# Kernel tuning notes

Measured on AMD Instinct MI355X. Metric: run time of the kernel, lower is better.

The kernel has to match this reference:

```python
import jax, jax.numpy as jnp
import numpy as np

N = 50000; E = 800000; IN = 64; HID = 128; H = 8; C = 16; G = 64
NEG = 0.2  # leaky_relu negative slope (GATv2 default and explicit in forward)

def _ln(x, g, b, eps=1e-5):
    mu = jnp.mean(x, -1, keepdims=True)
    var = jnp.var(x, -1, keepdims=True)
    return (x - mu) * jax.lax.rsqrt(var + eps) * g + b

def _prelu(x, a):
    return jnp.where(x >= 0, x, a * x)

def _gatv2(h, src, dst, Wl, bl, Wr, br, att, bias):
    # GATv2Conv: heads=H, out=C per head, concat=True, add_self_loops=True
    n = h.shape[0]
    loop = jnp.arange(n, dtype=src.dtype)
    s = jnp.concatenate([src, loop]); d = jnp.concatenate([dst, loop])
    xl = (h @ Wl + bl).reshape(n, H, C)   # source transform (messages)
    xr = (h @ Wr + br).reshape(n, H, C)   # target transform
    z = jax.nn.leaky_relu(xl[s] + xr[d], NEG)          # [Etot,H,C]
    e = jnp.einsum('ehc,hc->eh', z, att)               # [Etot,H]
    m = jax.ops.segment_max(e, d, num_segments=n)      # scatter-softmax over dst
    w = jnp.exp(e - m[d])
    denom = jax.ops.segment_sum(w, d, num_segments=n)
    alpha = w / (denom[d] + 1e-16)
    out = jax.ops.segment_sum(xl[s] * alpha[:, :, None], d, num_segments=n)
    return out.reshape(n, H * C) + bias

def _sage(h, src, dst, Wp, bp, Wl, bl, Wr):
    # SAGEConv(aggr='mean', normalize=True, project=True)
    n = h.shape[0]
    xp = jax.nn.relu(h @ Wp + bp)                      # project before aggregation
    summ = jax.ops.segment_sum(xp[src], dst, num_segments=n)
    cnt = jax.ops.segment_sum(jnp.ones_like(dst, dtype=h.dtype), dst, num_segments=n)
    mean = summ / jnp.maximum(cnt, 1.0)[:, None]
    out = mean @ Wl + bl + h @ Wr                      # root uses un-projected h
    nrm = jnp.linalg.norm(out, axis=-1, keepdims=True)
    return out / jnp.maximum(nrm, 1e-12)               # F.normalize(p=2, dim=-1)

def _forward(x, W_in, b_in, W_res, b_res,
             g0_Wl, g0_bl, g0_Wr, g0_br, g0_att, g0_bias,
             s1_Wp, s1_bp, s1_Wl, s1_bl, s1_Wr,
             g2_Wl, g2_bl, g2_Wr, g2_br, g2_att, g2_bias,
             s3_Wp, s3_bp, s3_Wl, s3_bl, s3_Wr,
             ln_g, ln_b, Wap, bap,
             Wc1, bc1, a1, Wc2, bc2, a2, Wc3, bc3,
             edge_index, batch):
    src, dst = edge_index[0], edge_index[1]
    h = (x @ W_in + b_in) + (x @ W_res + b_res)        # input_proj + res_proj
    xs0 = jax.nn.elu(_ln(_gatv2(h, src, dst, g0_Wl, g0_bl, g0_Wr, g0_br, g0_att, g0_bias), ln_g[0], ln_b[0]))
    xs1 = jax.nn.leaky_relu(_ln(_sage(xs0, src, dst, s1_Wp, s1_bp, s1_Wl, s1_bl, s1_Wr), ln_g[1], ln_b[1]), NEG)
    xs2 = jax.nn.elu(_ln(_gatv2(xs1, src, dst, g2_Wl, g2_bl, g2_Wr, g2_br, g2_att, g2_bias), ln_g[2], ln_b[2]))
    xs3 = jax.nn.leaky_relu(_ln(_sage(xs2, src, dst, s3_Wp, s3_bp, s3_Wl, s3_bl, s3_Wr), ln_g[3], ln_b[3]), NEG)
    h = jnp.maximum(jnp.maximum(xs0, xs1), jnp.maximum(xs2, xs3))  # JumpingKnowledge('max')
    att = jax.nn.sigmoid(h @ Wap + bap)
    h = h * att
    summ = jax.ops.segment_sum(h, batch, num_segments=G)
    cnt = jax.ops.segment_sum(jnp.ones((h.shape[0],), h.dtype), batch, num_segments=G)
    pooled = summ / jnp.maximum(cnt, 1.0)[:, None]     # global_mean_pool
    z = _prelu(pooled @ Wc1 + bc1, a1)
    z = _prelu(z @ Wc2 + bc2, a2)
    return z @ Wc3 + bc3

def setup_inputs():
    key = jax.random.key(0)
    ks = iter(jax.random.split(key, 64))
    def nrm(shape, fan):
        return jax.random.normal(next(ks), shape, jnp.float32) / np.sqrt(fan).astype(np.float32)
    inp = {}
    inp['x'] = jax.random.normal(next(ks), (N, IN), jnp.float32)
    inp['edge_index'] = jax.random.randint(next(ks), (2, E), 0, N, jnp.int32)
    inp['batch'] = jnp.sort(jax.random.randint(next(ks), (N,), 0, G, jnp.int32))
    inp['W_in'] = nrm((IN, HID), IN); inp['b_in'] = jnp.zeros((HID,))
    inp['W_res'] = nrm((IN, HID), IN); inp['b_res'] = jnp.zeros((HID,))
    for p in ('g0', 'g2'):
        inp[p + '_Wl'] = nrm((HID, HID), HID); inp[p + '_bl'] = jnp.zeros((HID,))
        inp[p + '_Wr'] = nrm((HID, HID), HID); inp[p + '_br'] = jnp.zeros((HID,))
        inp[p + '_att'] = nrm((H, C), C); inp[p + '_bias'] = jnp.zeros((HID,))
    for p in ('s1', 's3'):
        inp[p + '_Wp'] = nrm((HID, HID), HID); inp[p + '_bp'] = jnp.zeros((HID,))
        inp[p + '_Wl'] = nrm((HID, HID), HID); inp[p + '_bl'] = jnp.zeros((HID,))
        inp[p + '_Wr'] = nrm((HID, HID), HID)
    inp['ln_g'] = jnp.ones((4, HID)); inp['ln_b'] = jnp.zeros((4, HID))
    inp['Wap'] = nrm((HID, 1), HID); inp['bap'] = jnp.zeros((1,))
    inp['Wc1'] = nrm((HID, HID), HID); inp['bc1'] = jnp.zeros((HID,))
    inp['a1'] = jnp.float32(0.25)
    inp['Wc2'] = nrm((HID, HID // 2), HID); inp['bc2'] = jnp.zeros((HID // 2,))
    inp['a2'] = jnp.float32(0.25)
    inp['Wc3'] = nrm((HID // 2, 2), HID // 2); inp['bc3'] = jnp.zeros((2,))
    return inp

def reference(x, edge_index, batch, W_in, b_in, W_res, b_res,
              g0_Wl, g0_bl, g0_Wr, g0_br, g0_att, g0_bias,
              s1_Wp, s1_bp, s1_Wl, s1_bl, s1_Wr,
              g2_Wl, g2_bl, g2_Wr, g2_br, g2_att, g2_bias,
              s3_Wp, s3_bp, s3_Wl, s3_bl, s3_Wr,
              ln_g, ln_b, Wap, bap, Wc1, bc1, a1, Wc2, bc2, a2, Wc3, bc3):
    return _forward(x, W_in, b_in, W_res, b_res,
                    g0_Wl, g0_bl, g0_Wr, g0_br, g0_att, g0_bias,
                    s1_Wp, s1_bp, s1_Wl, s1_bl, s1_Wr,
                    g2_Wl, g2_bl, g2_Wr, g2_br, g2_att, g2_bias,
                    s3_Wp, s3_bp, s3_Wl, s3_bl, s3_Wr,
                    ln_g, ln_b, Wap, bap, Wc1, bc1, a1, Wc2, bc2, a2, Wc3, bc3,
                    edge_index, batch)
```

## Files before the change

kernel.cpp:

```cpp
#include <hip/hip_runtime.h>
#include <math.h>

constexpr int N_ = 50000;
constexpr int E_ = 800000;
constexpr int IN_ = 64;
constexpr int HID_ = 128;
constexpr int G_ = 64;
constexpr float NEG_ = 0.2f;
constexpr float LOG2E_ = 1.44269504088896340736f;

#define ACT_NONE 0
#define ACT_RELU 1

typedef _Float16 half8 __attribute__((ext_vector_type(8)));
typedef _Float16 half2v __attribute__((ext_vector_type(2)));
typedef float floatx4 __attribute__((ext_vector_type(4)));

__global__ __launch_bounds__(256) void hist_kernel(const int* __restrict__ dst,
                                                   int* __restrict__ deg, int e) {
  int i = blockIdx.x * 256 + threadIdx.x;
  if (i < e) atomicAdd(&deg[dst[i]], 1);
}

__global__ __launch_bounds__(256) void scan1_kernel(const int* __restrict__ deg,
                                                    int* __restrict__ excl,
                                                    int* __restrict__ bscan, int n) {
  __shared__ int sh[256];
  int t = threadIdx.x;
  int i = blockIdx.x * 256 + t;
  int v = (i < n) ? deg[i] : 0;
  sh[t] = v;
  __syncthreads();
  for (int off = 1; off < 256; off <<= 1) {
    int y = (t >= off) ? sh[t - off] : 0;
    __syncthreads();
    sh[t] += y;
    __syncthreads();
  }
  int incl = sh[t];
  if (i < n) excl[i] = incl - v;
  if (t == 255) bscan[blockIdx.x] = incl;
}

__global__ __launch_bounds__(256) void scan2_kernel(int* __restrict__ data, int nb) {
  __shared__ int sh[256];
  int t = threadIdx.x;
  int v = (t < nb) ? data[t] : 0;
  sh[t] = v;
  __syncthreads();
  for (int off = 1; off < 256; off <<= 1) {
    int y = (t >= off) ? sh[t - off] : 0;
    __syncthreads();
    sh[t] += y;
    __syncthreads();
  }
  if (t < nb) data[t] = sh[t] - v;
}

__global__ __launch_bounds__(256) void scan3_kernel(int* __restrict__ rowptr,
                                                    int* __restrict__ cursor,
                                                    const int* __restrict__ bscan,
                                                    int n, int e) {
  int i = blockIdx.x * 256 + threadIdx.x;
  if (i < n) {
    int v = rowptr[i] + bscan[blockIdx.x];
    rowptr[i] = v;
    cursor[i] = v;
  }
  if (i == n) rowptr[n] = e;
}

__global__ __launch_bounds__(256) void fill_kernel(const int* __restrict__ src,
                                                   const int* __restrict__ dst,
                                                   int* __restrict__ cursor,
                                                   int* __restrict__ csr, int e) {
  int i = blockIdx.x * 256 + threadIdx.x;
  if (i < e) {
    int d = dst[i];
    int p = atomicAdd(&cursor[d], 1);
    csr[p] = src[i];
  }
}

__global__ __launch_bounds__(256) void addv_kernel(const float* __restrict__ a,
                                                   const float* __restrict__ b,
                                                   float* __restrict__ o, int n) {
  int i = blockIdx.x * 256 + threadIdx.x;
  if (i < n) o[i] = a[i] + b[i];
}

__global__ __launch_bounds__(256) void prep_w_kernel(
    const float* __restrict__ W_in, const float* __restrict__ W_res,
    const float* __restrict__ m0, const float* __restrict__ m1,
    const float* __restrict__ m2, const float* __restrict__ m3,
    const float* __restrict__ m4, const float* __restrict__ m5,
    const float* __restrict__ m6, const float* __restrict__ m7,
    const float* __restrict__ m8, const float* __restrict__ m9,
    _Float16* __restrict__ dst) {
  int idx = blockIdx.x * 256 + threadIdx.x;
  if (idx < 8192) {
    int n = idx >> 6, k = idx & 63;
    float v = W_in[k * 128 + n] + W_res[k * 128 + n];
    _Float16 h = (_Float16)v;
    dst[idx] = h;
    dst[8192 + idx] = (_Float16)(v - (float)h);
  } else if (idx < 8192 + 10 * 16384) {
    int r = idx - 8192;
    int j = r >> 14;
    int e = r & 16383;
    int n = e >> 7, k = e & 127;
    const float* S;
    switch (j) {
      case 0: S = m0; break; case 1: S = m1; break; case 2: S = m2; break;
      case 3: S = m3; break; case 4: S = m4; break; case 5: S = m5; break;
      case 6: S = m6; break; case 7: S = m7; break; case 8: S = m8; break;
      default: S = m9; break;
    }
    float v = S[k * 128 + n];
    _Float16 h = (_Float16)v;
    _Float16* base = dst + 16384 + j * 32768;
    base[e] = h;
    base[16384 + e] = (_Float16)(v - (float)h);
  }
}

__device__ inline void split8v(float4 a, float4 b, half8& h, half8& l) {
  float v0 = a.x, v1 = a.y, v2 = a.z, v3 = a.w;
  float v4 = b.x, v5 = b.y, v6 = b.z, v7 = b.w;
  _Float16 h0 = (_Float16)v0, h1 = (_Float16)v1, h2 = (_Float16)v2, h3 = (_Float16)v3;
  _Float16 h4 = (_Float16)v4, h5 = (_Float16)v5, h6 = (_Float16)v6, h7 = (_Float16)v7;
  h[0] = h0; h[1] = h1; h[2] = h2; h[3] = h3; h[4] = h4; h[5] = h5; h[6] = h6; h[7] = h7;
  l[0] = (_Float16)(v0 - (float)h0); l[1] = (_Float16)(v1 - (float)h1);
  l[2] = (_Float16)(v2 - (float)h2); l[3] = (_Float16)(v3 - (float)h3);
  l[4] = (_Float16)(v4 - (float)h4); l[5] = (_Float16)(v5 - (float)h5);
  l[6] = (_Float16)(v6 - (float)h6); l[7] = (_Float16)(v7 - (float)h7);
}

template <int K1, int ACT, typename OutT>
__global__ __launch_bounds__(256, 2) void gemm_rw(const float* __restrict__ A,
                                                  const _Float16* __restrict__ Wh,
                                                  const _Float16* __restrict__ Wl,
                                                  const float* __restrict__ bias,
                                                  OutT* __restrict__ C, int M) {
  constexpr int KK = K1 / 32;
  const int t = threadIdx.x;
  const int wave = t >> 6, lane = t & 63;
  const int quad = lane >> 4, l16 = lane & 15;
  const int nt0 = wave * 2;

  half8 wh[2][KK], wl[2][KK];
  float bb[2];
  int col[2];
#pragma unroll
  for (int i = 0; i < 2; ++i) {
    col[i] = (nt0 + i) * 16 + l16;
    bb[i] = bias[col[i]];
#pragma unroll
    for (int k = 0; k < KK; ++k) {
      size_t off = (size_t)col[i] * K1 + k * 32 + quad * 8;
      wh[i][k] = *reinterpret_cast<const half8*>(Wh + off);
      wl[i][k] = *reinterpret_cast<const half8*>(Wl + off);
    }
  }
  const int r0 = blockIdx.x * 64;
#pragma unroll
  for (int tt = 0; tt < 4; ++tt) {
    int tb = r0 + tt * 16;
    if (tb >= M) break;
    int arow = tb + l16;
    if (arow >= M) arow = M - 1;
    const float* ap = A + (size_t)arow * K1 + quad * 8;
    float4 a0[KK], a1[KK];
#pragma unroll
    for (int k = 0; k < KK; ++k) {
      a0[k] = *reinterpret_cast<const float4*>(ap + k * 32);
      a1[k] = *reinterpret_cast<const float4*>(ap + k * 32 + 4);
    }
    floatx4 acc[2];
    acc[0] = (floatx4){0.f, 0.f, 0.f, 0.f};
    acc[1] = (floatx4){0.f, 0.f, 0.f, 0.f};
#pragma unroll
    for (int k = 0; k < KK; ++k) {
      half8 ah, al;
      split8v(a0[k], a1[k], ah, al);
      acc[0] = __builtin_amdgcn_mfma_f32_16x16x32_f16(ah, wh[0][k], acc[0], 0, 0, 0);
      acc[0] = __builtin_amdgcn_mfma_f32_16x16x32_f16(ah, wl[0][k], acc[0], 0, 0, 0);
      acc[0] = __builtin_amdgcn_mfma_f32_16x16x32_f16(al, wh[0][k], acc[0], 0, 0, 0);
      acc[1] = __builtin_amdgcn_mfma_f32_16x16x32_f16(ah, wh[1][k], acc[1], 0, 0, 0);
      acc[1] = __builtin_amdgcn_mfma_f32_16x16x32_f16(ah, wl[1][k], acc[1], 0, 0, 0);
      acc[1] = __builtin_amdgcn_mfma_f32_16x16x32_f16(al, wh[1][k], acc[1], 0, 0, 0);
    }
#pragma unroll
    for (int i = 0; i < 2; ++i) {
#pragma unroll
      for (int reg = 0; reg < 4; ++reg) {
        int r = tb + quad * 4 + reg;
        if (r < M) {
          float v = acc[i][reg] + bb[i];
          if (ACT == ACT_RELU) v = fmaxf(v, 0.f);
          C[(size_t)r * 128 + col[i]] = (OutT)v;
        }
      }
    }
  }
}

__global__ __launch_bounds__(256, 2) void gemm_rw_dual_gat(const float* __restrict__ A,
                                                           const _Float16* __restrict__ W0h,
                                                           const _Float16* __restrict__ W0l,
                                                           const _Float16* __restrict__ W1h,
                                                           const _Float16* __restrict__ W1l,
                                                           const float* __restrict__ b0,
                                                           const float* __restrict__ b1,
                                                           _Float16* __restrict__ C0,
                                                           _Float16* __restrict__ C1, int M) {
  const int t = threadIdx.x;
  const int wave = t >> 6, lane = t & 63;
  const int quad = lane >> 4, l16 = lane & 15;
  const int nt0 = wave * 2;

  half8 w0h[2][4], w0l[2][4], w1h[2][4], w1l[2][4];
  float bb0[2], bb1[2];
  int col[2];
#pragma unroll
  for (int i = 0; i < 2; ++i) {
    col[i] = (nt0 + i) * 16 + l16;
    bb0[i] = b0[col[i]];
    bb1[i] = b1[col[i]];
#pragma unroll
    for (int k = 0; k < 4; ++k) {
      size_t off = (size_t)col[i] * 128 + k * 32 + quad * 8;
      w0h[i][k] = *reinterpret_cast<const half8*>(W0h + off);
      w0l[i][k] = *reinterpret_cast<const half8*>(W0l + off);
      w1h[i][k] = *reinterpret_cast<const half8*>(W1h + off);
      w1l[i][k] = *reinterpret_cast<const half8*>(W1l + off);
    }
  }
  const int r0 = blockIdx.x * 64;
#pragma unroll
  for (int tt = 0; tt < 4; ++tt) {
    int tb = r0 + tt * 16;
    if (tb >= M) break;
    int arow = tb + l16;
    if (arow >= M) arow = M - 1;
    const float* ap = A + (size_t)arow * 128 + quad * 8;
    float4 a0[4], a1[4];
#pragma unroll
    for (int k = 0; k < 4; ++k) {
      a0[k] = *reinterpret_cast<const float4*>(ap + k * 32);
      a1[k] = *reinterpret_cast<const float4*>(ap + k * 32 + 4);
    }
    floatx4 acc0[2], acc1[2];
    acc0[0] = (floatx4){0.f, 0.f, 0.f, 0.f};
    acc0[1] = (floatx4){0.f, 0.f, 0.f, 0.f};
    acc1[0] = (floatx4){0.f, 0.f, 0.f, 0.f};
    acc1[1] = (floatx4){0.f, 0.f, 0.f, 0.f};
#pragma unroll
    for (int k = 0; k < 4; ++k) {
      half8 ah, al;
      split8v(a0[k], a1[k], ah, al);
#pragma unroll
      for (int i = 0; i < 2; ++i) {
        acc0[i] = __builtin_amdgcn_mfma_f32_16x16x32_f16(ah, w0h[i][k], acc0[i], 0, 0, 0);
        acc0[i] = __builtin_amdgcn_mfma_f32_16x16x32_f16(ah, w0l[i][k], acc0[i], 0, 0, 0);
        acc0[i] = __builtin_amdgcn_mfma_f32_16x16x32_f16(al, w0h[i][k], acc0[i], 0, 0, 0);
        acc1[i] = __builtin_amdgcn_mfma_f32_16x16x32_f16(ah, w1h[i][k], acc1[i], 0, 0, 0);
        acc1[i] = __builtin_amdgcn_mfma_f32_16x16x32_f16(ah, w1l[i][k], acc1[i], 0, 0, 0);
        acc1[i] = __builtin_amdgcn_mfma_f32_16x16x32_f16(al, w1h[i][k], acc1[i], 0, 0, 0);
      }
    }
#pragma unroll
    for (int i = 0; i < 2; ++i) {
#pragma unroll
      for (int reg = 0; reg < 4; ++reg) {
        int r = tb + quad * 4 + reg;
        if (r < M) {
          C0[(size_t)r * 128 + col[i]] = (_Float16)(acc0[i][reg] + bb0[i]);
          C1[(size_t)r * 128 + col[i]] = (_Float16)(acc1[i][reg] + bb1[i]);
        }
      }
    }
  }
}

__global__ __launch_bounds__(256, 2) void gemm_rw_dual_sage(const float* __restrict__ A1,
                                                            const _Float16* __restrict__ W1h,
                                                            const _Float16* __restrict__ W1l,
                                                            const float* __restrict__ A2,
                                                            const _Float16* __restrict__ W2h,
                                                            const _Float16* __restrict__ W2l,
                                                            const float* __restrict__ bias,
                                                            const float* __restrict__ lng,
                                                            const float* __restrict__ lnb,
                                                            float* __restrict__ C, int M) {
  const int t = threadIdx.x;
  const int wave = t >> 6, lane = t & 63;
  const int quad = lane >> 4, l16 = lane & 15;
  const int nt0 = wave * 2;

  half8 w1h[2][4], w1l[2][4], w2h[2][4], w2l[2][4];
  float bb[2], gg[2], lb[2];
  int col[2];
#pragma unroll
  for (int i = 0; i < 2; ++i) {
    col[i] = (nt0 + i) * 16 + l16;
    bb[i] = bias[col[i]];
    gg[i] = lng[col[i]];
    lb[i] = lnb[col[i]];
#pragma unroll
    for (int k = 0; k < 4; ++k) {
      size_t off = (size_t)col[i] * 128 + k * 32 + quad * 8;
      w1h[i][k] = *reinterpret_cast<const half8*>(W1h + off);
      w1l[i][k] = *reinterpret_cast<const half8*>(W1l + off);
      w2h[i][k] = *reinterpret_cast<const half8*>(W2h + off);
      w2l[i][k] = *reinterpret_cast<const half8*>(W2l + off);
    }
  }
  __shared__ float2 red[2][4][16];
  const int r0 = blockIdx.x * 64;
#pragma unroll 1
  for (int tt = 0; tt < 4; ++tt) {
    int tb = r0 + tt * 16;
    if (tb >= M) break;
    int arow = tb + l16;
    if (arow >= M) arow = M - 1;
    const float* ap1 = A1 + (size_t)arow * 128 + quad * 8;
    const float* ap2 = A2 + (size_t)arow * 128 + quad * 8;
    float4 a0[4], a1[4], c0[4], c1[4];
#pragma unroll
    for (int k = 0; k < 4; ++k) {
      a0[k] = *reinterpret_cast<const float4*>(ap1 + k * 32);
      a1[k] = *reinterpret_cast<const float4*>(ap1 + k * 32 + 4);
      c0[k] = *reinterpret_cast<const float4*>(ap2 + k * 32);
      c1[k] = *reinterpret_cast<const float4*>(ap2 + k * 32 + 4);
    }
    floatx4 acc[2];
    acc[0] = (floatx4){0.f, 0.f, 0.f, 0.f};
    acc[1] = (floatx4){0.f, 0.f, 0.f, 0.f};
#pragma unroll
    for (int k = 0; k < 4; ++k) {
      half8 ah, al;
      split8v(a0[k], a1[k], ah, al);
#pragma unroll
      for (int i = 0; i < 2; ++i) {
        acc[i] = __builtin_amdgcn_mfma_f32_16x16x32_f16(ah, w1h[i][k], acc[i], 0, 0, 0);
        acc[i] = __builtin_amdgcn_mfma_f32_16x16x32_f16(ah, w1l[i][k], acc[i], 0, 0, 0);
        acc[i] = __builtin_amdgcn_mfma_f32_16x16x32_f16(al, w1h[i][k], acc[i], 0, 0, 0);
      }
    }
#pragma unroll
    for (int k = 0; k < 4; ++k) {
      half8 ah, al;
      split8v(c0[k], c1[k], ah, al);
#pragma unroll
      for (int i = 0; i < 2; ++i) {
        acc[i] = __builtin_amdgcn_mfma_f32_16x16x32_f16(ah, w2h[i][k], acc[i], 0, 0, 0);
        acc[i] = __builtin_amdgcn_mfma_f32_16x16x32_f16(ah, w2l[i][k], acc[i], 0, 0, 0);
        acc[i] = __builtin_amdgcn_mfma_f32_16x16x32_f16(al, w2h[i][k], acc[i], 0, 0, 0);
      }
    }
    float v0[4], v1[4], p1[4], p2[4];
#pragma unroll
    for (int reg = 0; reg < 4; ++reg) {
      v0[reg] = acc[0][reg] + bb[0];
      v1[reg] = acc[1][reg] + bb[1];
      p1[reg] = v0[reg] + v1[reg];
      p2[reg] = v0[reg] * v0[reg] + v1[reg] * v1[reg];
    }
#pragma unroll
    for (int off = 1; off < 16; off <<= 1) {
#pragma unroll
      for (int reg = 0; reg < 4; ++reg) {
        p1[reg] += __shfl_xor(p1[reg], off, 64);
        p2[reg] += __shfl_xor(p2[reg], off, 64);
      }
    }
    int par = tt & 1;
    if (l16 == 0) {
#pragma unroll
      for (int reg = 0; reg < 4; ++reg)
        red[par][wave][quad * 4 + reg] = make_float2(p1[reg], p2[reg]);
    }
    __syncthreads();
#pragma unroll
    for (int reg = 0; reg < 4; ++reg) {
      int rr = quad * 4 + reg;
      float2 q0 = red[par][0][rr], q1 = red[par][1][rr];
      float2 q2 = red[par][2][rr], q3 = red[par][3][rr];
      float s1 = q0.x + q1.x + q2.x + q3.x;
      float s2 = q0.y + q1.y + q2.y + q3.y;
      float inv = 1.f / fmaxf(sqrtf(s2), 1e-12f);
      float mu = s1 * inv * (1.f / 128.f);
      float ex2 = (s2 * inv) * inv * (1.f / 128.f);
      float rstd = rsqrtf(ex2 - mu * mu + 1e-5f);
      int r = tb + rr;
      if (r < M) {
        float o0 = (v0[reg] * inv - mu) * rstd * gg[0] + lb[0];
        float o1 = (v1[reg] * inv - mu) * rstd * gg[1] + lb[1];
        o0 = fmaxf(o0, NEG_ * o0);
        o1 = fmaxf(o1, NEG_ * o1);
        C[(size_t)r * 128 + col[0]] = o0;
        C[(size_t)r * 128 + col[1]] = o1;
      }
    }
  }
}

__global__ __launch_bounds__(256) void gat_ln_kernel(const _Float16* __restrict__ xl,
                                                     const _Float16* __restrict__ xr,
                                                     const float* __restrict__ att,
                                                     const float* __restrict__ gbias,
                                                     const int* __restrict__ rowptr,
                                                     const int* __restrict__ csr,
                                                     const float* __restrict__ lng,
                                                     const float* __restrict__ lnb,
                                                     float* __restrict__ out, int n) {
  int wid = (blockIdx.x * 256 + threadIdx.x) >> 6;
  int lane = threadIdx.x & 63;
  if (wid >= n) return;
  const int h = lane >> 3, e = lane & 7;
  const char* __restrict__ xbase = (const char*)(xl + h * 16);

  half2v xr2[8], at2[8];
  {
    const uint4* xrp = reinterpret_cast<const uint4*>(xr + (size_t)wid * 128 + h * 16);
    uint4 u0 = xrp[0], u1 = xrp[1];
    unsigned uu[8] = {u0.x, u0.y, u0.z, u0.w, u1.x, u1.y, u1.z, u1.w};
#pragma unroll
    for (int i = 0; i < 8; ++i) xr2[i] = __builtin_bit_cast(half2v, uu[i]);
    const float2* ap = reinterpret_cast<const float2*>(att + h * 16);
#pragma unroll
    for (int i = 0; i < 8; ++i) {
      float2 a = ap[i];
      at2[i][0] = (_Float16)(a.x * LOG2E_);
      at2[i][1] = (_Float16)(a.y * LOG2E_);
    }
  }
  const half2v negc = {(_Float16)NEG_, (_Float16)NEG_};

  float m0, den;
  float acc[16];
  {
    const uint4* sp = reinterpret_cast<const uint4*>(xbase + (size_t)wid * 256);
    uint4 u0 = sp[0], u1 = sp[1];
    unsigned uu[8] = {u0.x, u0.y, u0.z, u0.w, u1.x, u1.y, u1.z, u1.w};
    float p = 0.f;
#pragma unroll
    for (int i = 0; i < 8; ++i) {
      half2v x = __builtin_bit_cast(half2v, uu[i]);
      half2v z = x + xr2[i];
      half2v zl = __builtin_elementwise_max(z, z * negc);
      p = __builtin_amdgcn_fdot2(zl, at2[i], p, false);
    }
    m0 = p;
    float w = (e == 0) ? 1.f : 0.f;
    den = w;
#pragma unroll
    for (int i = 0; i < 8; ++i) {
      half2v x = __builtin_bit_cast(half2v, uu[i]);
      acc[2 * i] = w * (float)x[0];
      acc[2 * i + 1] = w * (float)x[1];
    }
  }

  int beg = rowptr[wid], end = rowptr[wid + 1];
  for (int base = beg; base < end; base += 8) {
    int idx = base + e;
    bool valid = idx < end;
    int ci = valid ? idx : end - 1;
    int s = csr[ci];
    const uint4* gp = reinterpret_cast<const uint4*>(xbase + (size_t)s * 256);
    uint4 u0 = gp[0], u1 = gp[1];
    unsigned uu[8] = {u0.x, u0.y, u0.z, u0.w, u1.x, u1.y, u1.z, u1.w};
    float p = 0.f;
#pragma unroll
    for (int i = 0; i < 8; ++i) {
      half2v x = __builtin_bit_cast(half2v, uu[i]);
      half2v z = x + xr2[i];
      half2v zl = __builtin_elementwise_max(z, z * negc);
      p = __builtin_amdgcn_fdot2(zl, at2[i], p, false);
    }
    float w = valid ? exp2f(p - m0) : 0.f;
    den += w;
#pragma unroll
    for (int i = 0; i < 8; ++i) {
      half2v x = __builtin_bit_cast(half2v, uu[i]);
      acc[2 * i] += w * (float)x[0];
      acc[2 * i + 1] += w * (float)x[1];
    }
  }

#pragma unroll
  for (int off = 1; off < 8; off <<= 1) {
    den += __shfl_xor(den, off, 64);
#pragma unroll
    for (int i = 0; i < 16; ++i) acc[i] += __shfl_xor(acc[i], off, 64);
  }

  float inv = 1.f / (den + 1e-16f);
  int c = h * 16 + 2 * e;
  float2 bv = reinterpret_cast<const float2*>(gbias + c)[0];
  float o0 = acc[2 * e] * inv + bv.x;
  float o1 = acc[2 * e + 1] * inv + bv.y;
  float s1 = o0 + o1;
  float s2 = o0 * o0 + o1 * o1;
#pragma unroll
  for (int off = 1; off < 64; off <<= 1) {
    s1 += __shfl_xor(s1, off, 64);
    s2 += __shfl_xor(s2, off, 64);
  }
  float mu = s1 * (1.f / 128.f);
  float var = s2 * (1.f / 128.f) - mu * mu;
  float rstd = rsqrtf(var + 1e-5f);
  float2 gvv = reinterpret_cast<const float2*>(lng + c)[0];
  float2 lbv = reinterpret_cast<const float2*>(lnb + c)[0];
  float e0 = (o0 - mu) * rstd * gvv.x + lbv.x;
  float e1 = (o1 - mu) * rstd * gvv.y + lbv.y;
  e0 = e0 > 0.f ? e0 : exp2f(e0 * LOG2E_) - 1.f;
  e1 = e1 > 0.f ? e1 : exp2f(e1 * LOG2E_) - 1.f;
  *reinterpret_cast<float2*>(out + (size_t)wid * 128 + c) = make_float2(e0, e1);
}

__global__ __launch_bounds__(256) void sage_agg_kernel(const _Float16* __restrict__ xp,
                                                       const int* __restrict__ rowptr,
                                                       const int* __restrict__ csr,
                                                       float* __restrict__ mean, int n) {
  int wid = (blockIdx.x * 256 + threadIdx.x) >> 6;
  int lane = threadIdx.x & 63;
  if (wid >= n) return;
  const int g = lane >> 3, e = lane & 7;
  const char* __restrict__ xbase = (const char*)(xp + g * 16);

  float acc[16];
#pragma unroll
  for (int i = 0; i < 16; ++i) acc[i] = 0.f;

  int beg = rowptr[wid], end = rowptr[wid + 1];
  for (int base = beg; base < end; base += 8) {
    int idx = base + e;
    bool valid = idx < end;
    int ci = valid ? idx : end - 1;
    int s = csr[ci];
    const uint4* gp = reinterpret_cast<const uint4*>(xbase + (size_t)s * 256);
    uint4 u0 = gp[0], u1 = gp[1];
    unsigned uu[8] = {u0.x, u0.y, u0.z, u0.w, u1.x, u1.y, u1.z, u1.w};
    float w = valid ? 1.f : 0.f;
#pragma unroll
    for (int i = 0; i < 8; ++i) {
      half2v x = __builtin_bit_cast(half2v, uu[i]);
      acc[2 * i] += w * (float)x[0];
      acc[2 * i + 1] += w * (float)x[1];
    }
  }
#pragma unroll
  for (int off = 1; off < 8; off <<= 1) {
#pragma unroll
    for (int i = 0; i < 16; ++i) acc[i] += __shfl_xor(acc[i], off, 64);
  }
  float inv = 1.f / fmaxf((float)(end - beg), 1.f);
  int c = g * 16 + 2 * e;
  *reinterpret_cast<float2*>(mean + (size_t)wid * 128 + c) =
      make_float2(acc[2 * e] * inv, acc[2 * e + 1] * inv);
}

__global__ __launch_bounds__(256) void jk_pool_kernel(const float* __restrict__ x0,
                                                      const float* __restrict__ x1,
                                                      const float* __restrict__ x2,
                                                      const float* __restrict__ x3,
                                                      const float* __restrict__ wap,
                                                      const float* __restrict__ bap,
                                                      const int* __restrict__ batch,
                                                      float* __restrict__ pooled,
                                                      float* __restrict__ cnt, int n,
                                                      int chunk) {
  int wid = (blockIdx.x * 256 + threadIdx.x) >> 6;
  int lane = threadIdx.x & 63;
  int start = wid * chunk;
  if (start >= n) return;
  int end = start + chunk;
  if (end > n) end = n;

  const float2 wv = reinterpret_cast<const float2*>(wap)[lane];
  const float b0 = bap[0];

  int cur = -1;
  float2 acc = make_float2(0.f, 0.f);
  float c = 0.f;

  for (int i = start; i < end; ++i) {
    int off = i * 64 + lane;
    float2 a0 = reinterpret_cast<const float2*>(x0)[off];
    float2 a1 = reinterpret_cast<const float2*>(x1)[off];
    float2 a2 = reinterpret_cast<const float2*>(x2)[off];
    float2 a3 = reinterpret_cast<const float2*>(x3)[off];
    float2 v;
    v.x = fmaxf(fmaxf(a0.x, a1.x), fmaxf(a2.x, a3.x));
    v.y = fmaxf(fmaxf(a0.y, a1.y), fmaxf(a2.y, a3.y));
    float p = v.x * wv.x + v.y * wv.y;
#pragma unroll
    for (int o = 1; o < 64; o <<= 1) p += __shfl_xor(p, o, 64);
    float a = 1.f / (1.f + exp2f(-(p + b0) * LOG2E_));
    int bg = batch[i];
    if (bg != cur) {
      if (cur >= 0) {
        atomicAdd(&pooled[cur * 128 + 2 * lane], acc.x);
        atomicAdd(&pooled[cur * 128 + 2 * lane + 1], acc.y);
        if (lane == 0) atomicAdd(&cnt[cur], c);
      }
      cur = bg;
      acc = make_float2(0.f, 0.f);
      c = 0.f;
    }
    acc.x += v.x * a;
    acc.y += v.y * a;
    c += 1.f;
  }
  if (cur >= 0) {
    atomicAdd(&pooled[cur * 128 + 2 * lane], acc.x);
    atomicAdd(&pooled[cur * 128 + 2 * lane + 1], acc.y);
    if (lane == 0) atomicAdd(&cnt[cur], c);
  }
}

__global__ __launch_bounds__(128) void mlp_kernel(const float* __restrict__ pooled,
                                                  const float* __restrict__ cnt,
                                                  const float* __restrict__ Wc1,
                                                  const float* __restrict__ bc1,
                                                  const float* __restrict__ a1,
                                                  const float* __restrict__ Wc2,
                                                  const float* __restrict__ bc2,
                                                  const float* __restrict__ a2,
                                                  const float* __restrict__ Wc3,
                                                  const float* __restrict__ bc3,
                                                  float* __restrict__ out) {
  __shared__ float sh[128];
  __shared__ float sh2[128];
  __shared__ float sh3[64];
  int g = blockIdx.x, t = threadIdx.x;
  float inv = 1.f / fmaxf(cnt[g], 1.f);
  sh[t] = pooled[g * 128 + t] * inv;
  __syncthreads();
  float z = bc1[t];
  for (int k = 0; k < 128; ++k) z += sh[k] * Wc1[k * 128 + t];
  float al = a1[0];
  z = z >= 0.f ? z : al * z;
  sh2[t] = z;
  __syncthreads();
  if (t < 64) {
    float z2 = bc2[t];
    for (int k = 0; k < 128; ++k) z2 += sh2[k] * Wc2[k * 64 + t];
    float a2v = a2[0];
    z2 = z2 >= 0.f ? z2 : a2v * z2;
    sh3[t] = z2;
  }
  __syncthreads();
  if (t < 2) {
    float o = bc3[t];
    for (int k = 0; k < 64; ++k) o += sh3[k] * Wc3[k * 2 + t];
    out[g * 2 + t] = o;
  }
}

extern "C" void kernel_launch(void* const* d_in, const int* in_sizes, int n_in,
                              void* d_out, int out_size, void* d_ws, size_t ws_size,
                              hipStream_t stream) {
  const float* x = (const float*)d_in[0];
  const int* ei = (const int*)d_in[1];
  const int* batch = (const int*)d_in[2];
  const float* W_in = (const float*)d_in[3];
  const float* b_in = (const float*)d_in[4];
  const float* W_res = (const float*)d_in[5];
  const float* b_res = (const float*)d_in[6];
  const float* g0_Wl = (const float*)d_in[7];
  const float* g0_bl = (const float*)d_in[8];
  const float* g0_Wr = (const float*)d_in[9];
  const float* g0_br = (const float*)d_in[10];
  const float* g0_att = (const float*)d_in[11];
  const float* g0_bias = (const float*)d_in[12];
  const float* g2_Wl = (const float*)d_in[13];
  const float* g2_bl = (const float*)d_in[14];
  const float* g2_Wr = (const float*)d_in[15];
  const float* g2_br = (const float*)d_in[16];
  const float* g2_att = (const float*)d_in[17];
  const float* g2_bias = (const float*)d_in[18];
  const float* s1_Wp = (const float*)d_in[19];
  const float* s1_bp = (const float*)d_in[20];
  const float* s1_Wl = (const float*)d_in[21];
  const float* s1_bl = (const float*)d_in[22];
  const float* s1_Wr = (const float*)d_in[23];
  const float* s3_Wp = (const float*)d_in[24];
  const float* s3_bp = (const float*)d_in[25];
  const float* s3_Wl = (const float*)d_in[26];
  const float* s3_bl = (const float*)d_in[27];
  const float* s3_Wr = (const float*)d_in[28];
  const float* ln_g = (const float*)d_in[29];
  const float* ln_b = (const float*)d_in[30];
  const float* Wap = (const float*)d_in[31];
  const float* bap = (const float*)d_in[32];
  const float* Wc1 = (const float*)d_in[33];
  const float* bc1 = (const float*)d_in[34];
  const float* a1 = (const float*)d_in[35];
  const float* Wc2 = (const float*)d_in[36];
  const float* bc2 = (const float*)d_in[37];
  const float* a2 = (const float*)d_in[38];
  const float* Wc3 = (const float*)d_in[39];
  const float* bc3 = (const float*)d_in[40];
  float* out = (float*)d_out;

  char* w = (char*)d_ws;
  auto alloc = [&](size_t bytes) -> void* {
    void* p = (void*)w;
    w += (bytes + 255) & ~(size_t)255;
    return p;
  };
  int* deg_cursor = (int*)alloc((size_t)N_ * 4);
  int* rowptr = (int*)alloc((size_t)(N_ + 1) * 4);
  int* bscan = (int*)alloc(256 * 4);
  int* csr = (int*)alloc((size_t)E_ * 4);
  float* bsumf = (float*)alloc((size_t)HID_ * 4);
  float* pooled = (float*)alloc((size_t)G_ * HID_ * 4);
  float* cntf = (float*)alloc((size_t)G_ * 4);
  _Float16* wsp = (_Float16*)alloc((size_t)(16384 + 10 * 32768) * 2);
  size_t big = (size_t)N_ * HID_ * 4;
  size_t bigh = (size_t)N_ * HID_ * 2;
  float* T1 = (float*)alloc(big);
  float* T2 = (float*)alloc(big);
  _Float16* H0 = (_Float16*)alloc(bigh);
  _Float16* H1 = (_Float16*)alloc(bigh);
  float* B0 = (float*)alloc(big);
  float* B1 = (float*)alloc(big);
  float* B2 = (float*)alloc(big);
  float* B3 = (float*)alloc(big);

  const _Float16* WsT_h = wsp;
  const _Float16* WsT_l = wsp + 8192;
  auto WTh = [&](int j) { return (const _Float16*)(wsp + 16384 + j * 32768); };
  auto WTl = [&](int j) { return (const _Float16*)(wsp + 16384 + j * 32768 + 16384); };

  const int EB = (E_ + 255) / 256;
  const int NB256 = (N_ + 255) / 256;
  const int WB = (N_ + 3) / 4;
  const int GB = (N_ + 63) / 64;

  hipMemsetAsync(deg_cursor, 0, (size_t)N_ * 4, stream);
  hist_kernel<<<EB, 256, 0, stream>>>(ei + E_, deg_cursor, E_);
  scan1_kernel<<<NB256, 256, 0, stream>>>(deg_cursor, rowptr, bscan, N_);
  scan2_kernel<<<1, 256, 0, stream>>>(bscan, NB256);
  scan3_kernel<<<NB256, 256, 0, stream>>>(rowptr, deg_cursor, bscan, N_, E_);
  fill_kernel<<<EB, 256, 0, stream>>>(ei, ei + E_, deg_cursor, csr, E_);

  prep_w_kernel<<<(8192 + 10 * 16384 + 255) / 256, 256, 0, stream>>>(
      W_in, W_res, g0_Wl, g0_Wr, s1_Wp, s1_Wl, s1_Wr, g2_Wl, g2_Wr, s3_Wp, s3_Wl, s3_Wr, wsp);
  addv_kernel<<<1, 256, 0, stream>>>(b_in, b_res, bsumf, HID_);

  gemm_rw<64, ACT_NONE, float><<<GB, 256, 0, stream>>>(x, WsT_h, WsT_l, bsumf, T2, N_);

  gemm_rw_dual_gat<<<GB, 256, 0, stream>>>(T2, WTh(0), WTl(0), WTh(1), WTl(1), g0_bl, g0_br,
                                           H0, H1, N_);
  gat_ln_kernel<<<WB, 256, 0, stream>>>(H0, H1, g0_att, g0_bias, rowptr, csr,
                                        ln_g + 0 * 128, ln_b + 0 * 128, B0, N_);

  gemm_rw<128, ACT_RELU, _Float16><<<GB, 256, 0, stream>>>(B0, WTh(2), WTl(2), s1_bp, H0, N_);
  sage_agg_kernel<<<WB, 256, 0, stream>>>(H0, rowptr, csr, T1, N_);
  gemm_rw_dual_sage<<<GB, 256, 0, stream>>>(T1, WTh(3), WTl(3), B0, WTh(4), WTl(4), s1_bl,
                                            ln_g + 1 * 128, ln_b + 1 * 128, B1, N_);

  gemm_rw_dual_gat<<<GB, 256, 0, stream>>>(B1, WTh(5), WTl(5), WTh(6), WTl(6), g2_bl, g2_br,
                                           H0, H1, N_);
  gat_ln_kernel<<<WB, 256, 0, stream>>>(H0, H1, g2_att, g2_bias, rowptr, csr,
                                        ln_g + 2 * 128, ln_b + 2 * 128, B2, N_);

  gemm_rw<128, ACT_RELU, _Float16><<<GB, 256, 0, stream>>>(B2, WTh(7), WTl(7), s3_bp, H0, N_);
  sage_agg_kernel<<<WB, 256, 0, stream>>>(H0, rowptr, csr, T1, N_);
  gemm_rw_dual_sage<<<GB, 256, 0, stream>>>(T1, WTh(8), WTl(8), B2, WTh(9), WTl(9), s3_bl,
                                            ln_g + 3 * 128, ln_b + 3 * 128, B3, N_);

  hipMemsetAsync(pooled, 0, (size_t)G_ * HID_ * 4, stream);
  hipMemsetAsync(cntf, 0, (size_t)G_ * 4, stream);
  {
    const int chunk = 12;
    int nwaves = (N_ + chunk - 1) / chunk;
    int nblocks = (nwaves + 3) / 4;
    jk_pool_kernel<<<nblocks, 256, 0, stream>>>(B0, B1, B2, B3, Wap, bap, batch,
                                                pooled, cntf, N_, chunk);
  }
  mlp_kernel<<<G_, 128, 0, stream>>>(pooled, cntf, Wc1, bc1, a1, Wc2, bc2, a2, Wc3, bc3, out);
}
```

Baseline: 714.5 us.

## Store intermediate activations in fp16 and drop split-precision A operand in GEMMs

All intermediate node feature buffers (T1, T2, B0-B3) now hold fp16 instead of fp32. The GEMMs read fp16 A directly, so they skip the hi/lo split of A and issue two MFMAs per tile instead of three. The bias-add kernel is folded into the weight prep kernel, and the two memsets are merged into one, which assumes pooled and cntf sit next to each other in the allocation. This halves activation memory traffic and cuts MFMA work, at the cost of fp16 rounding of the activations, which may reduce accuracy.

```diff
diff --git a/kernel.cpp b/kernel.cpp
--- a/kernel.cpp
+++ b/kernel.cpp
@@ -82,21 +82,15 @@
   }
 }
 
-__global__ __launch_bounds__(256) void addv_kernel(const float* __restrict__ a,
-                                                   const float* __restrict__ b,
-                                                   float* __restrict__ o, int n) {
-  int i = blockIdx.x * 256 + threadIdx.x;
-  if (i < n) o[i] = a[i] + b[i];
-}
-
 __global__ __launch_bounds__(256) void prep_w_kernel(
     const float* __restrict__ W_in, const float* __restrict__ W_res,
+    const float* __restrict__ b_in, const float* __restrict__ b_res,
     const float* __restrict__ m0, const float* __restrict__ m1,
     const float* __restrict__ m2, const float* __restrict__ m3,
     const float* __restrict__ m4, const float* __restrict__ m5,
     const float* __restrict__ m6, const float* __restrict__ m7,
     const float* __restrict__ m8, const float* __restrict__ m9,
-    _Float16* __restrict__ dst) {
+    _Float16* __restrict__ dst, float* __restrict__ bsum) {
   int idx = blockIdx.x * 256 + threadIdx.x;
   if (idx < 8192) {
     int n = idx >> 6, k = idx & 63;
@@ -121,6 +115,9 @@
     _Float16* base = dst + 16384 + j * 32768;
     base[e] = h;
     base[16384 + e] = (_Float16)(v - (float)h);
+  } else if (idx < 8192 + 10 * 16384 + 128) {
+    int k = idx - (8192 + 10 * 16384);
+    bsum[k] = b_in[k] + b_res[k];
   }
 }
 
@@ -136,13 +133,12 @@
   l[6] = (_Float16)(v6 - (float)h6); l[7] = (_Float16)(v7 - (float)h7);
 }
 
-template <int K1, int ACT, typename OutT>
-__global__ __launch_bounds__(256, 2) void gemm_rw(const float* __restrict__ A,
-                                                  const _Float16* __restrict__ Wh,
-                                                  const _Float16* __restrict__ Wl,
-                                                  const float* __restrict__ bias,
-                                                  OutT* __restrict__ C, int M) {
-  constexpr int KK = K1 / 32;
+__global__ __launch_bounds__(256, 2) void gemm_rw_in(const float* __restrict__ A,
+                                                     const _Float16* __restrict__ Wh,
+                                                     const _Float16* __restrict__ Wl,
+                                                     const float* __restrict__ bias,
+                                                     _Float16* __restrict__ C, int M) {
+  constexpr int K1 = 64, KK = 2;
   const int t = threadIdx.x;
   const int wave = t >> 6, lane = t & 63;
   const int quad = lane >> 4, l16 = lane & 15;
@@ -170,25 +166,78 @@
     int arow = tb + l16;
     if (arow >= M) arow = M - 1;
     const float* ap = A + (size_t)arow * K1 + quad * 8;
-    float4 a0[KK], a1[KK];
-#pragma unroll
-    for (int k = 0; k < KK; ++k) {
-      a0[k] = *reinterpret_cast<const float4*>(ap + k * 32);
-      a1[k] = *reinterpret_cast<const float4*>(ap + k * 32 + 4);
-    }
     floatx4 acc[2];
     acc[0] = (floatx4){0.f, 0.f, 0.f, 0.f};
     acc[1] = (floatx4){0.f, 0.f, 0.f, 0.f};
 #pragma unroll
     for (int k = 0; k < KK; ++k) {
+      float4 a0 = *reinterpret_cast<const float4*>(ap + k * 32);
+      float4 a1 = *reinterpret_cast<const float4*>(ap + k * 32 + 4);
       half8 ah, al;
-      split8v(a0[k], a1[k], ah, al);
+      split8v(a0, a1, ah, al);
       acc[0] = __builtin_amdgcn_mfma_f32_16x16x32_f16(ah, wh[0][k], acc[0], 0, 0, 0);
       acc[0] = __builtin_amdgcn_mfma_f32_16x16x32_f16(ah, wl[0][k], acc[0], 0, 0, 0);
       acc[0] = __builtin_amdgcn_mfma_f32_16x16x32_f16(al, wh[0][k], acc[0], 0, 0, 0);
       acc[1] = __builtin_amdgcn_mfma_f32_16x16x32_f16(ah, wh[1][k], acc[1], 0, 0, 0);
       acc[1] = __builtin_amdgcn_mfma_f32_16x16x32_f16(ah, wl[1][k], acc[1], 0, 0, 0);
       acc[1] = __builtin_amdgcn_mfma_f32_16x16x32_f16(al, wh[1][k], acc[1], 0, 0, 0);
+    }
+#pragma unroll
+    for (int i = 0; i < 2; ++i) {
+#pragma unroll
+      for (int reg = 0; reg < 4; ++reg) {
+        int r = tb + quad * 4 + reg;
+        if (r < M) C[(size_t)r * 128 + col[i]] = (_Float16)(acc[i][reg] + bb[i]);
+      }
+    }
+  }
+}
+
+template <int ACT, typename OutT>
+__global__ __launch_bounds__(256, 2) void gemm_rw16(const _Float16* __restrict__ A,
+                                                    const _Float16* __restrict__ Wh,
+                                                    const _Float16* __restrict__ Wl,
+                                                    const float* __restrict__ bias,
+                                                    OutT* __restrict__ C, int M) {
+  const int t = threadIdx.x;
+  const int wave = t >> 6, lane = t & 63;
+  const int quad = lane >> 4, l16 = lane & 15;
+  const int nt0 = wave * 2;
+
+  half8 wh[2][4], wl[2][4];
+  float bb[2];
+  int col[2];
+#pragma unroll
+  for (int i = 0; i < 2; ++i) {
+    col[i] = (nt0 + i) * 16 + l16;
+    bb[i] = bias[col[i]];
+#pragma unroll
+    for (int k = 0; k < 4; ++k) {
+      size_t off = (size_t)col[i] * 128 + k * 32 + quad * 8;
+      wh[i][k] = *reinterpret_cast<const half8*>(Wh + off);
+      wl[i][k] = *reinterpret_cast<const half8*>(Wl + off);
+    }
+  }
+  const int r0 = blockIdx.x * 64;
+#pragma unroll
+  for (int tt = 0; tt < 4; ++tt) {
+    int tb = r0 + tt * 16;
+    if (tb >= M) break;
+    int arow = tb + l16;
+    if (arow >= M) arow = M - 1;
+    const _Float16* ap = A + (size_t)arow * 128 + quad * 8;
+    half8 a[4];
+#pragma unroll
+    for (int k = 0; k < 4; ++k) a[k] = *reinterpret_cast<const half8*>(ap + k * 32);
+    floatx4 acc[2];
+    acc[0] = (floatx4){0.f, 0.f, 0.f, 0.f};
+    acc[1] = (floatx4){0.f, 0.f, 0.f, 0.f};
+#pragma unroll
+    for (int k = 0; k < 4; ++k) {
+      acc[0] = __builtin_amdgcn_mfma_f32_16x16x32_f16(a[k], wh[0][k], acc[0], 0, 0, 0);
+      acc[0] = __builtin_amdgcn_mfma_f32_16x16x32_f16(a[k], wl[0][k], acc[0], 0, 0, 0);
+      acc[1] = __builtin_amdgcn_mfma_f32_16x16x32_f16(a[k], wh[1][k], acc[1], 0, 0, 0);
+      acc[1] = __builtin_amdgcn_mfma_f32_16x16x32_f16(a[k], wl[1][k], acc[1], 0, 0, 0);
     }
 #pragma unroll
     for (int i = 0; i < 2; ++i) {
@@ -205,15 +254,15 @@
   }
 }
 
-__global__ __launch_bounds__(256, 2) void gemm_rw_dual_gat(const float* __restrict__ A,
-                                                           const _Float16* __restrict__ W0h,
-                                                           const _Float16* __restrict__ W0l,
-                                                           const _Float16* __restrict__ W1h,
-                                                           const _Float16* __restrict__ W1l,
-                                                           const float* __restrict__ b0,
-                                                           const float* __restrict__ b1,
-                                                           _Float16* __restrict__ C0,
-                                                           _Float16* __restrict__ C1, int M) {
+__global__ __launch_bounds__(256, 2) void gemm_rw16_dual_gat(const _Float16* __restrict__ A,
+                                                             const _Float16* __restrict__ W0h,
+                                                             const _Float16* __restrict__ W0l,
+                                                             const _Float16* __restrict__ W1h,
+                                                             const _Float16* __restrict__ W1l,
+                                                             const float* __restrict__ b0,
+                                                             const float* __restrict__ b1,
+                                                             _Float16* __restrict__ C0,
+                                                             _Float16* __restrict__ C1, int M) {
   const int t = threadIdx.x;
   const int wave = t >> 6, lane = t & 63;
   const int quad = lane >> 4, l16 = lane & 15;
@@ -243,13 +292,10 @@
     if (tb >= M) break;
     int arow = tb + l16;
     if (arow >= M) arow = M - 1;
-    const float* ap = A + (size_t)arow * 128 + quad * 8;
-    float4 a0[4], a1[4];
-#pragma unroll
-    for (int k = 0; k < 4; ++k) {
-      a0[k] = *reinterpret_cast<const float4*>(ap + k * 32);
-      a1[k] = *reinterpret_cast<const float4*>(ap + k * 32 + 4);
-    }
+    const _Float16* ap = A + (size_t)arow * 128 + quad * 8;
+    half8 a[4];
+#pragma unroll
+    for (int k = 0; k < 4; ++k) a[k] = *reinterpret_cast<const half8*>(ap + k * 32);
     floatx4 acc0[2], acc1[2];
     acc0[0] = (floatx4){0.f, 0.f, 0.f, 0.f};
     acc0[1] = (floatx4){0.f, 0.f, 0.f, 0.f};
@@ -257,16 +303,12 @@
     acc1[1] = (floatx4){0.f, 0.f, 0.f, 0.f};
 #pragma unroll
     for (int k = 0; k < 4; ++k) {
-      half8 ah, al;
-      split8v(a0[k], a1[k], ah, al);
 #pragma unroll
       for (int i = 0; i < 2; ++i) {
-        acc0[i] = __builtin_amdgcn_mfma_f32_16x16x32_f16(ah, w0h[i][k], acc0[i], 0, 0, 0);
-        acc0[i] = __builtin_amdgcn_mfma_f32_16x16x32_f16(ah, w0l[i][k], acc0[i], 0, 0, 0);
-        acc0[i] = __builtin_amdgcn_mfma_f32_16x16x32_f16(al, w0h[i][k], acc0[i], 0, 0, 0);
-        acc1[i] = __builtin_amdgcn_mfma_f32_16x16x32_f16(ah, w1h[i][k], acc1[i], 0, 0, 0);
-        acc1[i] = __builtin_amdgcn_mfma_f32_16x16x32_f16(ah, w1l[i][k], acc1[i], 0, 0, 0);
-        acc1[i] = __builtin_amdgcn_mfma_f32_16x16x32_f16(al, w1h[i][k], acc1[i], 0, 0, 0);
+        acc0[i] = __builtin_amdgcn_mfma_f32_16x16x32_f16(a[k], w0h[i][k], acc0[i], 0, 0, 0);
+        acc0[i] = __builtin_amdgcn_mfma_f32_16x16x32_f16(a[k], w0l[i][k], acc0[i], 0, 0, 0);
+        acc1[i] = __builtin_amdgcn_mfma_f32_16x16x32_f16(a[k], w1h[i][k], acc1[i], 0, 0, 0);
+        acc1[i] = __builtin_amdgcn_mfma_f32_16x16x32_f16(a[k], w1l[i][k], acc1[i], 0, 0, 0);
       }
     }
 #pragma unroll
@@ -283,16 +325,16 @@
   }
 }
 
-__global__ __launch_bounds__(256, 2) void gemm_rw_dual_sage(const float* __restrict__ A1,
-                                                            const _Float16* __restrict__ W1h,
-                                                            const _Float16* __restrict__ W1l,
-                                                            const float* __restrict__ A2,
-                                                            const _Float16* __restrict__ W2h,
-                                                            const _Float16* __restrict__ W2l,
-                                                            const float* __restrict__ bias,
-                                                            const float* __restrict__ lng,
-                                                            const float* __restrict__ lnb,
-                                                            float* __restrict__ C, int M) {
+__global__ __launch_bounds__(256, 2) void gemm_rw16_dual_sage(const _Float16* __restrict__ A1,
+                                                              const _Float16* __restrict__ W1h,
+                                                              const _Float16* __restrict__ W1l,
+                                                              const _Float16* __restrict__ A2,
+                                                              const _Float16* __restrict__ W2h,
+                                                              const _Float16* __restrict__ W2l,
+                                                              const float* __restrict__ bias,
+                                                              const float* __restrict__ lng,
+                                                              const float* __restrict__ lnb,
+                                                              _Float16* __restrict__ C, int M) {
   const int t = threadIdx.x;
   const int wave = t >> 6, lane = t & 63;
   const int quad = lane >> 4, l16 = lane & 15;
@@ -324,39 +366,25 @@
     if (tb >= M) break;
     int arow = tb + l16;
     if (arow >= M) arow = M - 1;
-    const float* ap1 = A1 + (size_t)arow * 128 + quad * 8;
-    const float* ap2 = A2 + (size_t)arow * 128 + quad * 8;
-    float4 a0[4], a1[4], c0[4], c1[4];
+    const _Float16* ap1 = A1 + (size_t)arow * 128 + quad * 8;
+    const _Float16* ap2 = A2 + (size_t)arow * 128 + quad * 8;
+    half8 a[4], b[4];
 #pragma unroll
     for (int k = 0; k < 4; ++k) {
-      a0[k] = *reinterpret_cast<const float4*>(ap1 + k * 32);
-      a1[k] = *reinterpret_cast<const float4*>(ap1 + k * 32 + 4);
-      c0[k] = *reinterpret_cast<const float4*>(ap2 + k * 32);
-      c1[k] = *reinterpret_cast<const float4*>(ap2 + k * 32 + 4);
+      a[k] = *reinterpret_cast<const half8*>(ap1 + k * 32);
+      b[k] = *reinterpret_cast<const half8*>(ap2 + k * 32);
     }
     floatx4 acc[2];
     acc[0] = (floatx4){0.f, 0.f, 0.f, 0.f};
     acc[1] = (floatx4){0.f, 0.f, 0.f, 0.f};
 #pragma unroll
     for (int k = 0; k < 4; ++k) {
-      half8 ah, al;
-      split8v(a0[k], a1[k], ah, al);
 #pragma unroll
       for (int i = 0; i < 2; ++i) {
-        acc[i] = __builtin_amdgcn_mfma_f32_16x16x32_f16(ah, w1h[i][k], acc[i], 0, 0, 0);
-        acc[i] = __builtin_amdgcn_mfma_f32_16x16x32_f16(ah, w1l[i][k], acc[i], 0, 0, 0);
-        acc[i] = __builtin_amdgcn_mfma_f32_16x16x32_f16(al, w1h[i][k], acc[i], 0, 0, 0);
-      }
-    }
-#pragma unroll
-    for (int k = 0; k < 4; ++k) {
-      half8 ah, al;
-      split8v(c0[k], c1[k], ah, al);
-#pragma unroll
-      for (int i = 0; i < 2; ++i) {
-        acc[i] = __builtin_amdgcn_mfma_f32_16x16x32_f16(ah, w2h[i][k], acc[i], 0, 0, 0);
-        acc[i] = __builtin_amdgcn_mfma_f32_16x16x32_f16(ah, w2l[i][k], acc[i], 0, 0, 0);
-        acc[i] = __builtin_amdgcn_mfma_f32_16x16x32_f16(al, w2h[i][k], acc[i], 0, 0, 0);
+        acc[i] = __builtin_amdgcn_mfma_f32_16x16x32_f16(a[k], w1h[i][k], acc[i], 0, 0, 0);
+        acc[i] = __builtin_amdgcn_mfma_f32_16x16x32_f16(a[k], w1l[i][k], acc[i], 0, 0, 0);
+        acc[i] = __builtin_amdgcn_mfma_f32_16x16x32_f16(b[k], w2h[i][k], acc[i], 0, 0, 0);
+        acc[i] = __builtin_amdgcn_mfma_f32_16x16x32_f16(b[k], w2l[i][k], acc[i], 0, 0, 0);
       }
     }
     float v0[4], v1[4], p1[4], p2[4];
@@ -399,8 +427,8 @@
         float o1 = (v1[reg] * inv - mu) * rstd * gg[1] + lb[1];
         o0 = fmaxf(o0, NEG_ * o0);
         o1 = fmaxf(o1, NEG_ * o1);
-        C[(size_t)r * 128 + col[0]] = o0;
-        C[(size_t)r * 128 + col[1]] = o1;
+        C[(size_t)r * 128 + col[0]] = (_Float16)o0;
+        C[(size_t)r * 128 + col[1]] = (_Float16)o1;
       }
     }
   }
@@ -414,7 +442,7 @@
                                                      const int* __restrict__ csr,
                                                      const float* __restrict__ lng,
                                                      const float* __restrict__ lnb,
-                                                     float* __restrict__ out, int n) {
+                                                     _Float16* __restrict__ out, int n) {
   int wid = (blockIdx.x * 256 + threadIdx.x) >> 6;
   int lane = threadIdx.x & 63;
   if (wid >= n) return;
@@ -518,13 +546,16 @@
   float e1 = (o1 - mu) * rstd * gvv.y + lbv.y;
   e0 = e0 > 0.f ? e0 : exp2f(e0 * LOG2E_) - 1.f;
   e1 = e1 > 0.f ? e1 : exp2f(e1 * LOG2E_) - 1.f;
-  *reinterpret_cast<float2*>(out + (size_t)wid * 128 + c) = make_float2(e0, e1);
+  half2v o;
+  o[0] = (_Float16)e0;
+  o[1] = (_Float16)e1;
+  reinterpret_cast<half2v*>(out)[wid * 64 + (c >> 1)] = o;
 }
 
 __global__ __launch_bounds__(256) void sage_agg_kernel(const _Float16* __restrict__ xp,
                                                        const int* __restrict__ rowptr,
                                                        const int* __restrict__ csr,
-                                                       float* __restrict__ mean, int n) {
+                                                       _Float16* __restrict__ mean, int n) {
   int wid = (blockIdx.x * 256 + threadIdx.x) >> 6;
   int lane = threadIdx.x & 63;
   if (wid >= n) return;
@@ -559,14 +590,16 @@
   }
   float inv = 1.f / fmaxf((float)(end - beg), 1.f);
   int c = g * 16 + 2 * e;
-  *reinterpret_cast<float2*>(mean + (size_t)wid * 128 + c) =
-      make_float2(acc[2 * e] * inv, acc[2 * e + 1] * inv);
-}
-
-__global__ __launch_bounds__(256) void jk_pool_kernel(const float* __restrict__ x0,
-                                                      const float* __restrict__ x1,
-                                                      const float* __restrict__ x2,
-                                                      const float* __restrict__ x3,
+  half2v o;
+  o[0] = (_Float16)(acc[2 * e] * inv);
+  o[1] = (_Float16)(acc[2 * e + 1] * inv);
+  reinterpret_cast<half2v*>(mean)[wid * 64 + (c >> 1)] = o;
+}
+
+__global__ __launch_bounds__(256) void jk_pool_kernel(const _Float16* __restrict__ x0,
+                                                      const _Float16* __restrict__ x1,
+                                                      const _Float16* __restrict__ x2,
+                                                      const _Float16* __restrict__ x3,
                                                       const float* __restrict__ wap,
                                                       const float* __restrict__ bap,
                                                       const int* __restrict__ batch,
@@ -589,13 +622,14 @@
 
   for (int i = start; i < end; ++i) {
     int off = i * 64 + lane;
-    float2 a0 = reinterpret_cast<const float2*>(x0)[off];
-    float2 a1 = reinterpret_cast<const float2*>(x1)[off];
-    float2 a2 = reinterpret_cast<const float2*>(x2)[off];
-    float2 a3 = reinterpret_cast<const float2*>(x3)[off];
-    float2 v;
-    v.x = fmaxf(fmaxf(a0.x, a1.x), fmaxf(a2.x, a3.x));
-    v.y = fmaxf(fmaxf(a0.y, a1.y), fmaxf(a2.y, a3.y));
+    half2v a0 = reinterpret_cast<const half2v*>(x0)[off];
+    half2v a1 = reinterpret_cast<const half2v*>(x1)[off];
+    half2v a2 = reinterpret_cast<const half2v*>(x2)[off];
+    half2v a3 = reinterpret_cast<const half2v*>(x3)[off];
+    half2v m01 = __builtin_elementwise_max(a0, a1);
+    half2v m23 = __builtin_elementwise_max(a2, a3);
+    half2v mm = __builtin_elementwise_max(m01, m23);
+    float2 v = make_float2((float)mm[0], (float)mm[1]);
     float p = v.x * wv.x + v.y * wv.y;
 #pragma unroll
     for (int o = 1; o < 64; o <<= 1) p += __shfl_xor(p, o, 64);
@@ -721,16 +755,15 @@
   float* pooled = (float*)alloc((size_t)G_ * HID_ * 4);
   float* cntf = (float*)alloc((size_t)G_ * 4);
   _Float16* wsp = (_Float16*)alloc((size_t)(16384 + 10 * 32768) * 2);
-  size_t big = (size_t)N_ * HID_ * 4;
   size_t bigh = (size_t)N_ * HID_ * 2;
-  float* T1 = (float*)alloc(big);
-  float* T2 = (float*)alloc(big);
+  _Float16* T1 = (_Float16*)alloc(bigh);
+  _Float16* T2 = (_Float16*)alloc(bigh);
   _Float16* H0 = (_Float16*)alloc(bigh);
   _Float16* H1 = (_Float16*)alloc(bigh);
-  float* B0 = (float*)alloc(big);
-  float* B1 = (float*)alloc(big);
-  float* B2 = (float*)alloc(big);
-  float* B3 = (float*)alloc(big);
+  _Float16* B0 = (_Float16*)alloc(bigh);
+  _Float16* B1 = (_Float16*)alloc(bigh);
+  _Float16* B2 = (_Float16*)alloc(bigh);
+  _Float16* B3 = (_Float16*)alloc(bigh);
 
   const _Float16* WsT_h = wsp;
   const _Float16* WsT_l = wsp + 8192;
@@ -749,34 +782,33 @@
   scan3_kernel<<<NB256, 256, 0, stream>>>(rowptr, deg_cursor, bscan, N_, E_);
   fill_kernel<<<EB, 256, 0, stream>>>(ei, ei + E_, deg_cursor, csr, E_);
 
-  prep_w_kernel<<<(8192 + 10 * 16384 + 255) / 256, 256, 0, stream>>>(
-      W_in, W_res, g0_Wl, g0_Wr, s1_Wp, s1_Wl, s1_Wr, g2_Wl, g2_Wr, s3_Wp, s3_Wl, s3_Wr, wsp);
-  addv_kernel<<<1, 256, 0, stream>>>(b_in, b_res, bsumf, HID_);
-
-  gemm_rw<64, ACT_NONE, float><<<GB, 256, 0, stream>>>(x, WsT_h, WsT_l, bsumf, T2, N_);
-
-  gemm_rw_dual_gat<<<GB, 256, 0, stream>>>(T2, WTh(0), WTl(0), WTh(1), WTl(1), g0_bl, g0_br,
-                                           H0, H1, N_);
+  prep_w_kernel<<<(8192 + 10 * 16384 + 128 + 255) / 256, 256, 0, stream>>>(
+      W_in, W_res, b_in, b_res, g0_Wl, g0_Wr, s1_Wp, s1_Wl, s1_Wr, g2_Wl, g2_Wr, s3_Wp,
+      s3_Wl, s3_Wr, wsp, bsumf);
+
+  gemm_rw_in<<<GB, 256, 0, stream>>>(x, WsT_h, WsT_l, bsumf, T2, N_);
+
+  gemm_rw16_dual_gat<<<GB, 256, 0, stream>>>(T2, WTh(0), WTl(0), WTh(1), WTl(1), g0_bl,
+                                             g0_br, H0, H1, N_);
   gat_ln_kernel<<<WB, 256, 0, stream>>>(H0, H1, g0_att, g0_bias, rowptr, csr,
                                         ln_g + 0 * 128, ln_b + 0 * 128, B0, N_);
 
-  gemm_rw<128, ACT_RELU, _Float16><<<GB, 256, 0, stream>>>(B0, WTh(2), WTl(2), s1_bp, H0, N_);
+  gemm_rw16<ACT_RELU, _Float16><<<GB, 256, 0, stream>>>(B0, WTh(2), WTl(2), s1_bp, H0, N_);
   sage_agg_kernel<<<WB, 256, 0, stream>>>(H0, rowptr, csr, T1, N_);
-  gemm_rw_dual_sage<<<GB, 256, 0, stream>>>(T1, WTh(3), WTl(3), B0, WTh(4), WTl(4), s1_bl,
-                                            ln_g + 1 * 128, ln_b + 1 * 128, B1, N_);
-
-  gemm_rw_dual_gat<<<GB, 256, 0, stream>>>(B1, WTh(5), WTl(5), WTh(6), WTl(6), g2_bl, g2_br,
-                                           H0, H1, N_);
+  gemm_rw16_dual_sage<<<GB, 256, 0, stream>>>(T1, WTh(3), WTl(3), B0, WTh(4), WTl(4), s1_bl,
+                                              ln_g + 1 * 128, ln_b + 1 * 128, B1, N_);
+
+  gemm_rw16_dual_gat<<<GB, 256, 0, stream>>>(B1, WTh(5), WTl(5), WTh(6), WTl(6), g2_bl,
+                                             g2_br, H0, H1, N_);
   gat_ln_kernel<<<WB, 256, 0, stream>>>(H0, H1, g2_att, g2_bias, rowptr, csr,
                                         ln_g + 2 * 128, ln_b + 2 * 128, B2, N_);
 
-  gemm_rw<128, ACT_RELU, _Float16><<<GB, 256, 0, stream>>>(B2, WTh(7), WTl(7), s3_bp, H0, N_);
+  gemm_rw16<ACT_RELU, _Float16><<<GB, 256, 0, stream>>>(B2, WTh(7), WTl(7), s3_bp, H0, N_);
   sage_agg_kernel<<<WB, 256, 0, stream>>>(H0, rowptr, csr, T1, N_);
-  gemm_rw_dual_sage<<<GB, 256, 0, stream>>>(T1, WTh(8), WTl(8), B2, WTh(9), WTl(9), s3_bl,
-                                            ln_g + 3 * 128, ln_b + 3 * 128, B3, N_);
-
-  hipMemsetAsync(pooled, 0, (size_t)G_ * HID_ * 4, stream);
-  hipMemsetAsync(cntf, 0, (size_t)G_ * 4, stream);
+  gemm_rw16_dual_sage<<<GB, 256, 0, stream>>>(T1, WTh(8), WTl(8), B2, WTh(9), WTl(9), s3_bl,
+                                              ln_g + 3 * 128, ln_b + 3 * 128, B3, N_);
+
+  hipMemsetAsync(pooled, 0, (size_t)G_ * HID_ * 4 + (size_t)G_ * 4, stream);
   {
     const int chunk = 12;
     int nwaves = (N_ + chunk - 1) / chunk;
```

Result: faster. 642.6 us, median of 2 (-10.1%).
